# Kernel tuning notes

Hardware: AMD Instinct MI355X
Metric: run time of the kernel (lower is better)

Reference implementation:

```python
import jax, jax.numpy as jnp
import numpy as np

WS, OWS, HEADS, DIM = 16, 24, 6, 192
PAD = (OWS - WS) // 2
NQ, NKV = WS * WS, OWS * OWS
TABLE = (WS + OWS - 1) ** 2


def _rpi():
    # replicates WindowsHandling.get_relative_position_index_for_overlap_window
    c = np.arange(WS)
    ori = np.stack(np.meshgrid(c, c, indexing='ij')).reshape(2, -1)
    e = np.arange(OWS)
    ext = np.stack(np.meshgrid(e, e, indexing='ij')).reshape(2, -1)
    rc = (ext[:, None, :] - ori[:, :, None]).transpose(1, 2, 0).astype(np.int64)
    rc[..., 0] += WS - OWS + 1
    rc[..., 1] += WS - OWS + 1
    rc[..., 0] *= WS + OWS - 1
    # mod mimics torch's negative advanced-index wraparound into the table
    return (rc.sum(-1) % TABLE).astype(np.int32)  # (NQ, NKV)


def _extract_patches(xp, nh, nw):
    # torch.nn.Unfold(kernel=OWS, stride=WS) equivalent on NHWC input.
    # xp: (b, PH, PW, c) -> (b*nh*nw, OWS*OWS, c), row-major window order.
    b, PH, PW, c = xp.shape
    i = (np.arange(nh) * WS)[:, None] + np.arange(OWS)[None, :]
    j = (np.arange(nw) * WS)[:, None] + np.arange(OWS)[None, :]
    t = jnp.take(xp, jnp.asarray(i.reshape(-1)), axis=1).reshape(b, nh, OWS, PW, c)
    t = jnp.take(t, jnp.asarray(j.reshape(-1)), axis=3).reshape(b, nh, OWS, nw, OWS, c)
    return t.transpose(0, 1, 3, 2, 4, 5).reshape(b * nh * nw, OWS * OWS, c)


def _attn_mask(h, w):
    # shift_size == 0 branch of get_attention_mask_for_overlap_window:
    # kv positions falling into the zero padding get -100.
    vm = np.zeros((1, h + 2 * PAD, w + 2 * PAD, 1), np.float32)
    vm[:, PAD:-PAD, PAD:-PAD, :] = 1.0
    nh, nw = h // WS, w // WS
    kv = np.asarray(_extract_patches(jnp.asarray(vm), nh, nw)).reshape(nh * nw, NKV)
    m = np.where(kv[:, None, :] > 0, 0.0, -100.0).astype(np.float32)
    return np.broadcast_to(m, (nh * nw, NQ, NKV)).copy()


def setup_inputs():
    key = jax.random.key(0)
    ks = jax.random.split(key, 8)
    b, h, w = 2, 160, 160
    s = 0.02
    return {
        'x': jax.random.normal(ks[0], (b, h, w, DIM), jnp.float32),
        'rpi': jnp.asarray(_rpi()),
        'attn_mask': jnp.asarray(_attn_mask(h, w)),
        'q_w': jax.random.normal(ks[1], (DIM, DIM), jnp.float32) * s,
        'q_b': jnp.zeros((DIM,), jnp.float32),
        'kv_w': jax.random.normal(ks[2], (DIM, 2 * DIM), jnp.float32) * s,
        'kv_b': jnp.zeros((2 * DIM,), jnp.float32),
        'bias_table': jax.random.normal(ks[3], (TABLE, HEADS), jnp.float32) * s,
        'gating_w': jax.random.normal(ks[4], (DIM, DIM), jnp.float32) * s,
        'gating_b': jnp.ones((DIM,), jnp.float32),
        'proj_w': jax.random.normal(ks[5], (DIM, DIM), jnp.float32) * s,
        'proj_b': jnp.zeros((DIM,), jnp.float32),
    }


def reference(x, rpi, attn_mask, q_w, q_b, kv_w, kv_b, bias_table, gating_w, gating_b, proj_w, proj_b):
    b, h, w, c = x.shape
    d = c // HEADS
    scale = d ** -0.5
    nh, nw = h // WS, w // WS
    nwin = nh * nw
    # shift_size == 0 path: zero-pad for overlapping kv windows
    x_pad = jnp.pad(x, ((0, 0), (PAD, PAD), (PAD, PAD), (0, 0)))
    # q windows (non-overlapping window partition)
    xw = x.reshape(b, nh, WS, nw, WS, c).transpose(0, 1, 3, 2, 4, 5).reshape(b * nwin, NQ, c)
    # kv windows (overlapping, Unfold equivalent)
    xpw = _extract_patches(x_pad, nh, nw)  # (b*nwin, NKV, c)
    gates = xw @ gating_w + gating_b                       # (b*nwin, NQ, c)
    q = (xw @ q_w + q_b).reshape(-1, NQ, HEADS, d).transpose(0, 2, 1, 3) * scale
    kv = xpw @ kv_w + kv_b
    k = kv[..., :c].reshape(-1, NKV, HEADS, d).transpose(0, 2, 1, 3)
    v = kv[..., c:].reshape(-1, NKV, HEADS, d).transpose(0, 2, 1, 3)
    attn = jnp.einsum('bhqd,bhkd->bhqk', q, k)             # (b*nwin, H, NQ, NKV)
    bias = bias_table[rpi.reshape(-1)].reshape(NQ, NKV, HEADS).transpose(2, 0, 1)
    attn = attn + bias[None]
    attn = attn.reshape(b, nwin, HEADS, NQ, NKV) + attn_mask[None, :, None]
    attn = jax.nn.softmax(attn, axis=-1).reshape(b * nwin, HEADS, NQ, NKV)
    out = jnp.einsum('bhqk,bhkd->bhqd', attn, v).transpose(0, 2, 1, 3).reshape(-1, NQ, c)
    out = out * gates
    out = out.reshape(b, nh, nw, WS, WS, c).transpose(0, 1, 3, 2, 4, 5).reshape(b, h, w, c)
    return out @ proj_w + proj_b
```

## Files before the change

kernel.cpp:

```cpp
#include <hip/hip_runtime.h>
#include <hip/hip_bf16.h>
#include <stdint.h>

typedef __bf16 bf16x8  __attribute__((ext_vector_type(8)));
typedef __bf16 bf16x4  __attribute__((ext_vector_type(4)));
typedef __bf16 bf16x16 __attribute__((ext_vector_type(16)));
typedef float  f32x4   __attribute__((ext_vector_type(4)));
typedef float  f32x16  __attribute__((ext_vector_type(16)));
typedef uint32_t u32;

#define MFMA16(a, b, c) __builtin_amdgcn_mfma_f32_16x16x32_bf16((a), (b), (c), 0, 0, 0)
#define MFMA32(a, b, c) __builtin_amdgcn_mfma_f32_32x32x16_bf16((a), (b), (c), 0, 0, 0)

constexpr int CH = 160, CW = 160, CC = 192, CHEADS = 6, CD = 32;
constexpr int CNQ = 256, CNKV = 576, CPH = 168;
constexpr float LOG2E = 1.44269504088896340736f;
constexpr float QSCALE_L2E = 0.17677669529663687f * 1.44269504088896340736f;

__global__ __launch_bounds__(256)
void prep_k(const int* __restrict__ rpi, const float* __restrict__ tab,
            const float* __restrict__ q_w, const float* __restrict__ g_w,
            const float* __restrict__ kv_w, const float* __restrict__ p_w,
            const float* __restrict__ q_b, const float* __restrict__ g_b,
            const float* __restrict__ kv_b, const float* __restrict__ p_b,
            __bf16* __restrict__ BTh, u32* __restrict__ mt,
            __bf16* __restrict__ Wt, __bf16* __restrict__ Wp,
            float* __restrict__ b768, float* __restrict__ pb,
            __bf16* __restrict__ KVb)
{
    const int bidg = blockIdx.x;
    if (bidg < 216) {
        int idx = bidg * 256 + threadIdx.x;
        int lane = idx & 63;
        int rest = idx >> 6;
        int ktg = rest % 18; rest /= 18;
        int qtg = rest & 7;
        int head = rest >> 3;
        int l31 = lane & 31, hi = lane >> 5;
        int q = qtg * 32 + l31;
        bf16x16 o16;
#pragma unroll
        for (int g = 0; g < 4; ++g) {
            int4 ri = *(const int4*)(rpi + q * CNKV + ktg * 32 + 4 * hi + g * 8);
            o16[g * 4 + 0] = (__bf16)(tab[ri.x * CHEADS + head] * LOG2E);
            o16[g * 4 + 1] = (__bf16)(tab[ri.y * CHEADS + head] * LOG2E);
            o16[g * 4 + 2] = (__bf16)(tab[ri.z * CHEADS + head] * LOG2E);
            o16[g * 4 + 3] = (__bf16)(tab[ri.w * CHEADS + head] * LOG2E);
        }
        *(bf16x16*)(BTh + (long)idx * 16) = o16;
    } else if (bidg < 257) {
        int idx = (bidg - 216) * 256 + threadIdx.x;
        if (idx >= 9 * 18 * 64) return;
        int lane = idx & 63;
        int rest = idx >> 6;
        int ktg = rest % 18;
        int cls = rest / 18;
        int cy = cls / 3, cx = cls % 3;
        int hi = lane >> 5;
        u32 m = 0;
#pragma unroll
        for (int r = 0; r < 16; ++r) {
            int kv = ktg * 32 + 4 * hi + (r & 3) + 8 * (r >> 2);
            int oy = kv / 24, ox = kv - oy * 24;
            bool vy = (cy == 0) ? (oy >= 4) : ((cy == 2) ? (oy < 20) : true);
            bool vx = (cx == 0) ? (ox >= 4) : ((cx == 2) ? (ox < 20) : true);
            if (vy && vx) m |= (1u << r);
        }
        mt[idx] = m;
    } else if (bidg < 981) {
        int idx = (bidg - 257) * 256 + threadIdx.x;
        if (idx < 147456) {
            int n = idx / 192, k = idx - n * 192;
            float v;
            if (n < 192)      v = q_w[k * 192 + n] * QSCALE_L2E;
            else if (n < 384) v = g_w[k * 192 + (n - 192)];
            else              v = kv_w[k * 384 + (n - 384)];
            Wt[idx] = (__bf16)v;
        } else if (idx < 184320) {
            int j = idx - 147456;
            int n = j / 192, k = j - n * 192;
            Wp[j] = (__bf16)p_w[k * 192 + n];
        } else if (idx < 185280) {
            int j = idx - 184320;
            if (j < 192)      b768[j] = q_b[j] * QSCALE_L2E;
            else if (j < 384) b768[j] = g_b[j - 192];
            else if (j < 768) b768[j] = kv_b[j - 384];
            else              pb[j - 768] = p_b[j - 768];
        }
    } else {
        int tid = (bidg - 981) * 256 + threadIdx.x;
        if (tid >= 251904) return;
        int row = tid / 48, seg = tid - row * 48;
        int bb = row / 2624, rr = row - bb * 2624;
        int py, px;
        if (rr < 672)       { py = rr / 168;               px = rr % 168; }
        else if (rr < 1344) { int r2 = rr - 672; py = 164 + r2 / 168; px = r2 % 168; }
        else                { int rm = rr - 1344; py = 4 + rm / 8; int q = rm & 7;
                              px = (q < 4) ? q : 160 + q; }
        bf16x8 v;
#pragma unroll
        for (int j = 0; j < 8; ++j) v[j] = (__bf16)kv_b[seg * 8 + j];
        *(bf16x8*)(KVb + ((long)((bb * CPH + py) * CPH + px)) * 384 + seg * 8) = v;
    }
}

__global__ __launch_bounds__(256)
void gemm_f_k(const float* __restrict__ x, const __bf16* __restrict__ Wt,
              const float* __restrict__ b768,
              __bf16* __restrict__ Qb, __bf16* __restrict__ Gb,
              __bf16* __restrict__ KVb)
{
    __shared__ __bf16 As[2][4096];
    __shared__ __bf16 Bs[2][4096];

    const int bid = blockIdx.x;
    const int v = (bid & 7) * 1200 + (bid >> 3);
    const int bm = v / 12, bn = v - bm * 12;

    const int t = threadIdx.x, lane = t & 63, wv = t >> 6;
    const int l15 = lane & 15, l4 = lane >> 4;
    const int row = t >> 2, gp = t & 3;
    const int swz = row & 7;
    const int d0 = row * 64 + ((2 * gp) ^ swz) * 8;
    const int d1 = row * 64 + ((2 * gp + 1) ^ swz) * 8;

    const float*  asrc = x  + (long)(bm * 64 + row) * 192 + gp * 16;
    const __bf16* bsrc = Wt + (long)(bn * 64 + row) * 192 + gp * 16;

    float4 fa0, fa1, fa2, fa3;
    bf16x8 wb0, wb1;
    auto ld = [&](int kt) {
        const float* a = asrc + kt * 64;
        fa0 = ((const float4*)a)[0]; fa1 = ((const float4*)a)[1];
        fa2 = ((const float4*)a)[2]; fa3 = ((const float4*)a)[3];
        wb0 = *(const bf16x8*)(bsrc + kt * 64);
        wb1 = *(const bf16x8*)(bsrc + kt * 64 + 8);
    };
    auto st = [&](int buf) {
        bf16x8 g0, g1;
        g0[0] = (__bf16)fa0.x; g0[1] = (__bf16)fa0.y; g0[2] = (__bf16)fa0.z; g0[3] = (__bf16)fa0.w;
        g0[4] = (__bf16)fa1.x; g0[5] = (__bf16)fa1.y; g0[6] = (__bf16)fa1.z; g0[7] = (__bf16)fa1.w;
        g1[0] = (__bf16)fa2.x; g1[1] = (__bf16)fa2.y; g1[2] = (__bf16)fa2.z; g1[3] = (__bf16)fa2.w;
        g1[4] = (__bf16)fa3.x; g1[5] = (__bf16)fa3.y; g1[6] = (__bf16)fa3.z; g1[7] = (__bf16)fa3.w;
        *(bf16x8*)&As[buf][d0] = g0;
        *(bf16x8*)&As[buf][d1] = g1;
        *(bf16x8*)&Bs[buf][d0] = wb0;
        *(bf16x8*)&Bs[buf][d1] = wb1;
    };

    const int qm = (wv >> 1) * 32, qn = (wv & 1) * 32;
    f32x4 acc[2][2];
#pragma unroll
    for (int i = 0; i < 2; ++i)
#pragma unroll
        for (int j = 0; j < 2; ++j) acc[i][j] = f32x4{0.f, 0.f, 0.f, 0.f};

    ld(0);
    for (int kt = 0; kt < 3; ++kt) {
        const int buf = kt & 1;
        st(buf);
        if (kt < 2) ld(kt + 1);
        __syncthreads();
#pragma unroll
        for (int s = 0; s < 2; ++s) {
            bf16x8 af[2], bfr[2];
#pragma unroll
            for (int mi = 0; mi < 2; ++mi)
                af[mi] = *(const bf16x8*)&As[buf][(qm + mi * 16 + l15) * 64 +
                                                 (((s * 4 + l4) ^ (l15 & 7)) * 8)];
#pragma unroll
            for (int ni = 0; ni < 2; ++ni)
                bfr[ni] = *(const bf16x8*)&Bs[buf][(qn + ni * 16 + l15) * 64 +
                                                   (((s * 4 + l4) ^ (l15 & 7)) * 8)];
#pragma unroll
            for (int mi = 0; mi < 2; ++mi)
#pragma unroll
                for (int ni = 0; ni < 2; ++ni)
                    acc[mi][ni] = MFMA16(af[mi], bfr[ni], acc[mi][ni]);
        }
        __syncthreads();
    }

    __bf16* epi = &As[0][0];
    float bv0 = b768[bn * 64 + qn + l15];
    float bv1 = b768[bn * 64 + qn + 16 + l15];
#pragma unroll
    for (int mi = 0; mi < 2; ++mi)
#pragma unroll
        for (int ni = 0; ni < 2; ++ni)
#pragma unroll
            for (int r = 0; r < 4; ++r) {
                int rowl = qm + mi * 16 + l4 * 4 + r;
                int coll = qn + ni * 16 + l15;
                epi[rowl * 80 + coll] =
                    (__bf16)(acc[mi][ni][r] + (ni ? bv1 : bv0));
            }
    __syncthreads();
#pragma unroll
    for (int k = 0; k < 2; ++k) {
        int rid = t * 2 + k;
        int rowl = rid >> 3, seg = rid & 7;
        bf16x8 vv = *(const bf16x8*)&epi[rowl * 80 + seg * 8];
        int rowg = bm * 64 + rowl;
        int bb = rowg / 25600, rr = rowg - bb * 25600;
        int y = rr / 160, xx = rr - y * 160;
        int cg = bn * 64 + seg * 8;
        if (bn < 6) {
            int win = bb * 100 + (y >> 4) * 10 + (xx >> 4);
            long widx = ((long)win * 256 + (y & 15) * 16 + (xx & 15)) * 192;
            if (bn < 3) *(bf16x8*)(Qb + widx + cg) = vv;
            else        *(bf16x8*)(Gb + widx + cg - 192) = vv;
        } else {
            long kidx = ((long)((bb * CPH + y + 4) * CPH + (xx + 4))) * 384;
            *(bf16x8*)(KVb + kidx + cg - 384) = vv;
        }
    }
}

__global__ __launch_bounds__(256)
void gemm_p_k(const __bf16* __restrict__ Yb, const __bf16* __restrict__ Wp,
              const float* __restrict__ pb, float* __restrict__ of)
{
    __shared__ __bf16 As[2][4096];
    __shared__ __bf16 Bs[2][4096];

    const int bid = blockIdx.x;
    const int v = (bid & 7) * 300 + (bid >> 3);
    const int bm = v / 3, bn = v - bm * 3;

    const int t = threadIdx.x, lane = t & 63, wv = t >> 6;
    const int l15 = lane & 15, l4 = lane >> 4;
    const int row = t >> 2, gp = t & 3;
    const int swz = row & 7;
    const int d0 = row * 64 + ((2 * gp) ^ swz) * 8;
    const int d1 = row * 64 + ((2 * gp + 1) ^ swz) * 8;

    const __bf16* asrc = Yb + (long)(bm * 64 + row) * 192 + gp * 16;
    const __bf16* bsrc = Wp + (long)(bn * 64 + row) * 192 + gp * 16;

    bf16x8 a0, a1, wb0, wb1;
    auto ld = [&](int kt) {
        a0  = *(const bf16x8*)(asrc + kt * 64);
        a1  = *(const bf16x8*)(asrc + kt * 64 + 8);
        wb0 = *(const bf16x8*)(bsrc + kt * 64);
        wb1 = *(const bf16x8*)(bsrc + kt * 64 + 8);
    };
    auto st = [&](int buf) {
        *(bf16x8*)&As[buf][d0] = a0;
        *(bf16x8*)&As[buf][d1] = a1;
        *(bf16x8*)&Bs[buf][d0] = wb0;
        *(bf16x8*)&Bs[buf][d1] = wb1;
    };

    const int qm = (wv >> 1) * 32, qn = (wv & 1) * 32;
    f32x4 acc[2][2];
#pragma unroll
    for (int i = 0; i < 2; ++i)
#pragma unroll
        for (int j = 0; j < 2; ++j) acc[i][j] = f32x4{0.f, 0.f, 0.f, 0.f};

    ld(0);
    for (int kt = 0; kt < 3; ++kt) {
        const int buf = kt & 1;
        st(buf);
        if (kt < 2) ld(kt + 1);
        __syncthreads();
#pragma unroll
        for (int s = 0; s < 2; ++s) {
            bf16x8 af[2], bfr[2];
#pragma unroll
            for (int mi = 0; mi < 2; ++mi)
                af[mi] = *(const bf16x8*)&As[buf][(qm + mi * 16 + l15) * 64 +
                                                 (((s * 4 + l4) ^ (l15 & 7)) * 8)];
#pragma unroll
            for (int ni = 0; ni < 2; ++ni)
                bfr[ni] = *(const bf16x8*)&Bs[buf][(qn + ni * 16 + l15) * 64 +
                                                   (((s * 4 + l4) ^ (l15 & 7)) * 8)];
#pragma unroll
            for (int mi = 0; mi < 2; ++mi)
#pragma unroll
                for (int ni = 0; ni < 2; ++ni)
                    acc[mi][ni] = MFMA16(af[mi], bfr[ni], acc[mi][ni]);
        }
        __syncthreads();
    }

#pragma unroll
    for (int mi = 0; mi < 2; ++mi) {
#pragma unroll
        for (int r = 0; r < 4; ++r) {
            int rowg = bm * 64 + qm + mi * 16 + l4 * 4 + r;
            int win = rowg >> 8, q = rowg & 255;
            int bb = win / 100, wr = win % 100;
            int y = (wr / 10) * 16 + (q >> 4), xx = (wr % 10) * 16 + (q & 15);
            long oidx = ((long)((bb * CH + y) * CW + xx)) * 192;
#pragma unroll
            for (int ni = 0; ni < 2; ++ni) {
                int cg = bn * 64 + qn + ni * 16 + l15;
                of[oidx + cg] = acc[mi][ni][r] + pb[cg];
            }
        }
    }
}

__global__ __launch_bounds__(512, 4)
void attn12_k(const __bf16* __restrict__ Q, const __bf16* __restrict__ KV,
              const __bf16* __restrict__ G, const __bf16* __restrict__ BTh,
              const u32* __restrict__ MT, __bf16* __restrict__ Y)
{
    __shared__ __bf16 Ks[576][36];
    __shared__ __bf16 Vt[32][580];

    const int bid = blockIdx.x;
    const int xs = bid & 7, ii = bid >> 3;
    const int win = xs * 25 + ii / 6;
    const int head = ii % 6;

    const int bb = win / 100, wr = win % 100, wy = wr / 10, wx = wr % 10;
    const int cy = (wy == 0) ? 0 : ((wy == 9) ? 2 : 1);
    const int cx = (wx == 0) ? 0 : ((wx == 9) ? 2 : 1);
    const int cls = cy * 3 + cx;
    const int t = threadIdx.x, lane = t & 63, wv = t >> 6;
    const int l31 = lane & 31, hi = lane >> 5;

    {
        const int pos0 = t >> 3, seg = t & 7;
        int oy = pos0 / 24, ox = pos0 - oy * 24;
        const long rowbase = ((long)((bb * CPH + wy * 16) * CPH + wx * 16)) * 384
                             + head * CD;
        int pos = pos0;
#pragma unroll
        for (int r = 0; r < 9; ++r) {
            const __bf16* p = KV + rowbase + (long)(oy * CPH + ox) * 384;
            if (seg < 4) {
                bf16x8 k8 = *(const bf16x8*)(p + seg * 8);
                *(bf16x8*)&Ks[pos][seg * 8] = k8;
            } else {
                bf16x8 v8 = *(const bf16x8*)(p + 192 + (seg - 4) * 8);
#pragma unroll
                for (int j = 0; j < 8; ++j) Vt[(seg - 4) * 8 + j][pos] = v8[j];
            }
            pos += 64;
            oy += 2; ox += 16;
            if (ox >= 24) { ox -= 24; oy += 1; }
        }
    }

    bf16x8 qf0, qf1;
    {
        const __bf16* qb = Q + ((long)win * CNQ + wv * 32 + l31) * CC + head * CD;
        qf0 = *(const bf16x8*)(qb + hi * 8);
        qf1 = *(const bf16x8*)(qb + 16 + hi * 8);
    }
    const __bf16* btb = BTh + (long)((head * 8 + wv) * 18) * 1024 + (long)lane * 16;
    bf16x16 bA = *(const bf16x16*)btb;

    __syncthreads();

    f32x16 o = {};
    float srun = 0.f;

    const char* kbase = (const char*)&Ks[0][0] + l31 * 72 + hi * 16;
    const char* vbase = (const char*)&Vt[0][0] + l31 * 1160 + hi * 8;

    bf16x8 kc0 = *(const bf16x8*)(kbase);
    bf16x8 kc1 = *(const bf16x8*)(kbase + 32);
    f32x16 stv_cur;
#pragma unroll
    for (int r = 0; r < 16; ++r) stv_cur[r] = (float)bA[r];
    __builtin_amdgcn_s_setprio(1);
    stv_cur = MFMA32(kc0, qf0, stv_cur);
    stv_cur = MFMA32(kc1, qf1, stv_cur);
    __builtin_amdgcn_s_setprio(0);
    kc0 = *(const bf16x8*)(kbase + 2304);
    kc1 = *(const bf16x8*)(kbase + 2304 + 32);
    bA  = *(const bf16x16*)(btb + 1024);

    for (int tt = 0; tt < 18; ++tt) {
        f32x16 stv_next;
        if (tt < 17) {
#pragma unroll
            for (int r = 0; r < 16; ++r) stv_next[r] = (float)bA[r];
            __builtin_amdgcn_s_setprio(1);
            stv_next = MFMA32(kc0, qf0, stv_next);
            stv_next = MFMA32(kc1, qf1, stv_next);
            __builtin_amdgcn_s_setprio(0);
            if (tt < 16) {
                const char* kn = kbase + (tt + 2) * 2304;
                kc0 = *(const bf16x8*)(kn);
                kc1 = *(const bf16x8*)(kn + 32);
                bA  = *(const bf16x16*)(btb + (long)(tt + 2) * 1024);
            }
        }

        const char* vp = vbase + tt * 64;
        bf16x4 v0 = *(const bf16x4*)(vp);
        bf16x4 v1 = *(const bf16x4*)(vp + 16);
        bf16x4 v2 = *(const bf16x4*)(vp + 32);
        bf16x4 v3 = *(const bf16x4*)(vp + 48);
        bf16x8 vf0, vf1;
#pragma unroll
        for (int j = 0; j < 4; ++j) {
            vf0[j] = v0[j]; vf0[4 + j] = v1[j];
            vf1[j] = v2[j]; vf1[4 + j] = v3[j];
        }

        const bool needm = (cx != 1) || (cy == 0 && tt < 3) || (cy == 2 && tt >= 15);
        u32 m = 0xFFFFFFFFu;
        if (needm) m = MT[(cls * 18 + tt) * 64 + lane];

        float p[16];
#pragma unroll
        for (int r = 0; r < 16; ++r) p[r] = exp2f(stv_cur[r]);
        if (needm) {
#pragma unroll
            for (int r = 0; r < 16; ++r)
                p[r] = (m & (1u << r)) ? p[r] : 0.0f;
        }
        float s = 0.f;
#pragma unroll
        for (int r = 0; r < 16; ++r) s += p[r];
        srun += s;

        bf16x8 pa0, pa1;
#pragma unroll
        for (int j = 0; j < 8; ++j) {
            pa0[j] = (__bf16)p[j];
            pa1[j] = (__bf16)p[8 + j];
        }

        __builtin_amdgcn_s_setprio(1);
        o = MFMA32(vf0, pa0, o);
        o = MFMA32(vf1, pa1, o);
        __builtin_amdgcn_s_setprio(0);

        if (tt < 17) stv_cur = stv_next;
    }

    srun += __shfl_xor(srun, 32);
    float rs = 1.0f / srun;
    long base = ((long)win * CNQ + wv * 32 + l31) * CC + head * CD;
    const __bf16* gp2 = G + base;
    __bf16* yp = Y + base;
#pragma unroll
    for (int g = 0; g < 4; ++g) {
        bf16x4 gv = *(const bf16x4*)(gp2 + g * 8 + 4 * hi);
        bf16x4 ov;
#pragma unroll
        for (int j = 0; j < 4; ++j)
            ov[j] = (__bf16)(o[g * 4 + j] * rs * (float)gv[j]);
        *(bf16x4*)(yp + g * 8 + 4 * hi) = ov;
    }
}

extern "C" void kernel_launch(void* const* d_in, const int* in_sizes, int n_in,
                              void* d_out, int out_size, void* d_ws, size_t ws_size,
                              hipStream_t stream)
{
    (void)in_sizes; (void)n_in; (void)out_size; (void)ws_size;
    const float* x    = (const float*)d_in[0];
    const int*   rpi  = (const int*)  d_in[1];
    const float* q_w  = (const float*)d_in[3];
    const float* q_b  = (const float*)d_in[4];
    const float* kv_w = (const float*)d_in[5];
    const float* kv_b = (const float*)d_in[6];
    const float* btab = (const float*)d_in[7];
    const float* g_w  = (const float*)d_in[8];
    const float* g_b  = (const float*)d_in[9];
    const float* p_w  = (const float*)d_in[10];
    const float* p_b  = (const float*)d_in[11];
    float* out = (float*)d_out;

    char* ws = (char*)d_ws;
    __bf16* Qb  = (__bf16*)(ws);
    __bf16* KVb = (__bf16*)(ws + 19660800);
    __bf16* Gb  = (__bf16*)(ws + 63012864);
    __bf16* Yb  = (__bf16*)(ws + 82673664);
    __bf16* BTh = (__bf16*)(ws + 102334464);
    u32*    MT  = (u32*)   (ws + 104103936);
    __bf16* Wt  = (__bf16*)(ws + 104145408);
    __bf16* Wp  = (__bf16*)(ws + 104440320);
    float*  b768= (float*) (ws + 104514048);
    float*  pb  = (float*) (ws + 104517120);

    prep_k<<<1965, 256, 0, stream>>>(rpi, btab, q_w, g_w, kv_w, p_w,
                                     q_b, g_b, kv_b, p_b,
                                     BTh, MT, Wt, Wp, b768, pb, KVb);
    gemm_f_k<<<9600, 256, 0, stream>>>(x, Wt, b768, Qb, Gb, KVb);
    attn12_k<<<1200, 512, 0, stream>>>(Qb, KVb, Gb, BTh, MT, Yb);
    gemm_p_k<<<2400, 256, 0, stream>>>(Yb, Wp, pb, out);
}
```

Before: 144.8 us.

## Enlarge fused GEMM M-tile, restructure attention loop, sum probabilities via MFMA

The fused Q/gate/KV projection GEMM now uses 128x64 tiles instead of 64x64, halving the block count and increasing reuse of the weight tile per block. The attention kernel drops the one-step-ahead score pipelining in favour of prefetching only the next K and bias loads. Row sums of the probabilities are now accumulated with extra MFMAs against a ones vector instead of scalar adds plus a cross-lane shuffle. exp2f is swapped for the hardware builtin when available. The changes add register pressure and extra MFMA work, and may expose score latency that the old pipelining hid.

```diff
diff --git a/kernel.cpp b/kernel.cpp
--- a/kernel.cpp
+++ b/kernel.cpp
@@ -11,6 +11,12 @@
 
 #define MFMA16(a, b, c) __builtin_amdgcn_mfma_f32_16x16x32_bf16((a), (b), (c), 0, 0, 0)
 #define MFMA32(a, b, c) __builtin_amdgcn_mfma_f32_32x32x16_bf16((a), (b), (c), 0, 0, 0)
+
+#if __has_builtin(__builtin_amdgcn_exp2f)
+#define EXP2F(x) __builtin_amdgcn_exp2f(x)
+#else
+#define EXP2F(x) exp2f(x)
+#endif
 
 constexpr int CH = 160, CW = 160, CC = 192, CHEADS = 6, CD = 32;
 constexpr int CNQ = 256, CNKV = 576, CPH = 168;
@@ -110,48 +116,51 @@
               __bf16* __restrict__ Qb, __bf16* __restrict__ Gb,
               __bf16* __restrict__ KVb)
 {
-    __shared__ __bf16 As[2][4096];
+    __shared__ __bf16 As[2][8192];
     __shared__ __bf16 Bs[2][4096];
 
     const int bid = blockIdx.x;
-    const int v = (bid & 7) * 1200 + (bid >> 3);
+    const int v = (bid & 7) * 600 + (bid >> 3);
     const int bm = v / 12, bn = v - bm * 12;
 
     const int t = threadIdx.x, lane = t & 63, wv = t >> 6;
     const int l15 = lane & 15, l4 = lane >> 4;
-    const int row = t >> 2, gp = t & 3;
-    const int swz = row & 7;
-    const int d0 = row * 64 + ((2 * gp) ^ swz) * 8;
-    const int d1 = row * 64 + ((2 * gp + 1) ^ swz) * 8;
-
-    const float*  asrc = x  + (long)(bm * 64 + row) * 192 + gp * 16;
-    const __bf16* bsrc = Wt + (long)(bn * 64 + row) * 192 + gp * 16;
-
-    float4 fa0, fa1, fa2, fa3;
+    const int wm = wv >> 1, wn = wv & 1;
+
+    const int arow = t >> 1, ahalf = t & 1;
+    const int aswz = arow & 7;
+    const int brow = t >> 2, bgp = t & 3;
+    const int bswz = brow & 7;
+
+    const float*  asrc = x  + (long)(bm * 128 + arow) * 192 + ahalf * 32;
+    const __bf16* bsrc = Wt + (long)(bn * 64 + brow) * 192 + bgp * 16;
+
+    float4 fa[8];
     bf16x8 wb0, wb1;
     auto ld = [&](int kt) {
         const float* a = asrc + kt * 64;
-        fa0 = ((const float4*)a)[0]; fa1 = ((const float4*)a)[1];
-        fa2 = ((const float4*)a)[2]; fa3 = ((const float4*)a)[3];
+#pragma unroll
+        for (int q = 0; q < 8; ++q) fa[q] = ((const float4*)a)[q];
         wb0 = *(const bf16x8*)(bsrc + kt * 64);
         wb1 = *(const bf16x8*)(bsrc + kt * 64 + 8);
     };
     auto st = [&](int buf) {
-        bf16x8 g0, g1;
-        g0[0] = (__bf16)fa0.x; g0[1] = (__bf16)fa0.y; g0[2] = (__bf16)fa0.z; g0[3] = (__bf16)fa0.w;
-        g0[4] = (__bf16)fa1.x; g0[5] = (__bf16)fa1.y; g0[6] = (__bf16)fa1.z; g0[7] = (__bf16)fa1.w;
-        g1[0] = (__bf16)fa2.x; g1[1] = (__bf16)fa2.y; g1[2] = (__bf16)fa2.z; g1[3] = (__bf16)fa2.w;
-        g1[4] = (__bf16)fa3.x; g1[5] = (__bf16)fa3.y; g1[6] = (__bf16)fa3.z; g1[7] = (__bf16)fa3.w;
-        *(bf16x8*)&As[buf][d0] = g0;
-        *(bf16x8*)&As[buf][d1] = g1;
-        *(bf16x8*)&Bs[buf][d0] = wb0;
-        *(bf16x8*)&Bs[buf][d1] = wb1;
+#pragma unroll
+        for (int c = 0; c < 4; ++c) {
+            bf16x8 g;
+            g[0] = (__bf16)fa[2 * c].x; g[1] = (__bf16)fa[2 * c].y;
+            g[2] = (__bf16)fa[2 * c].z; g[3] = (__bf16)fa[2 * c].w;
+            g[4] = (__bf16)fa[2 * c + 1].x; g[5] = (__bf16)fa[2 * c + 1].y;
+            g[6] = (__bf16)fa[2 * c + 1].z; g[7] = (__bf16)fa[2 * c + 1].w;
+            *(bf16x8*)&As[buf][arow * 64 + ((ahalf * 4 + c) ^ aswz) * 8] = g;
+        }
+        *(bf16x8*)&Bs[buf][brow * 64 + ((2 * bgp) ^ bswz) * 8] = wb0;
+        *(bf16x8*)&Bs[buf][brow * 64 + ((2 * bgp + 1) ^ bswz) * 8] = wb1;
     };
 
-    const int qm = (wv >> 1) * 32, qn = (wv & 1) * 32;
-    f32x4 acc[2][2];
-#pragma unroll
-    for (int i = 0; i < 2; ++i)
+    f32x4 acc[4][2];
+#pragma unroll
+    for (int i = 0; i < 4; ++i)
 #pragma unroll
         for (int j = 0; j < 2; ++j) acc[i][j] = f32x4{0.f, 0.f, 0.f, 0.f};
 
@@ -163,17 +172,17 @@
         __syncthreads();
 #pragma unroll
         for (int s = 0; s < 2; ++s) {
-            bf16x8 af[2], bfr[2];
-#pragma unroll
-            for (int mi = 0; mi < 2; ++mi)
-                af[mi] = *(const bf16x8*)&As[buf][(qm + mi * 16 + l15) * 64 +
+            bf16x8 af[4], bfr[2];
+#pragma unroll
+            for (int mi = 0; mi < 4; ++mi)
+                af[mi] = *(const bf16x8*)&As[buf][(wm * 64 + mi * 16 + l15) * 64 +
                                                  (((s * 4 + l4) ^ (l15 & 7)) * 8)];
 #pragma unroll
             for (int ni = 0; ni < 2; ++ni)
-                bfr[ni] = *(const bf16x8*)&Bs[buf][(qn + ni * 16 + l15) * 64 +
+                bfr[ni] = *(const bf16x8*)&Bs[buf][(wn * 32 + ni * 16 + l15) * 64 +
                                                    (((s * 4 + l4) ^ (l15 & 7)) * 8)];
 #pragma unroll
-            for (int mi = 0; mi < 2; ++mi)
+            for (int mi = 0; mi < 4; ++mi)
 #pragma unroll
                 for (int ni = 0; ni < 2; ++ni)
                     acc[mi][ni] = MFMA16(af[mi], bfr[ni], acc[mi][ni]);
@@ -182,26 +191,26 @@
     }
 
     __bf16* epi = &As[0][0];
-    float bv0 = b768[bn * 64 + qn + l15];
-    float bv1 = b768[bn * 64 + qn + 16 + l15];
-#pragma unroll
-    for (int mi = 0; mi < 2; ++mi)
+    float bv0 = b768[bn * 64 + wn * 32 + l15];
+    float bv1 = b768[bn * 64 + wn * 32 + 16 + l15];
+#pragma unroll
+    for (int mi = 0; mi < 4; ++mi)
 #pragma unroll
         for (int ni = 0; ni < 2; ++ni)
 #pragma unroll
             for (int r = 0; r < 4; ++r) {
-                int rowl = qm + mi * 16 + l4 * 4 + r;
-                int coll = qn + ni * 16 + l15;
+                int rowl = wm * 64 + mi * 16 + l4 * 4 + r;
+                int coll = wn * 32 + ni * 16 + l15;
                 epi[rowl * 80 + coll] =
                     (__bf16)(acc[mi][ni][r] + (ni ? bv1 : bv0));
             }
     __syncthreads();
 #pragma unroll
-    for (int k = 0; k < 2; ++k) {
-        int rid = t * 2 + k;
+    for (int k = 0; k < 4; ++k) {
+        int rid = k * 256 + t;
         int rowl = rid >> 3, seg = rid & 7;
         bf16x8 vv = *(const bf16x8*)&epi[rowl * 80 + seg * 8];
-        int rowg = bm * 64 + rowl;
+        int rowg = bm * 128 + rowl;
         int bb = rowg / 25600, rr = rowg - bb * 25600;
         int y = rr / 160, xx = rr - y * 160;
         int cg = bn * 64 + seg * 8;
@@ -304,7 +313,7 @@
 }
 
 __global__ __launch_bounds__(512, 4)
-void attn12_k(const __bf16* __restrict__ Q, const __bf16* __restrict__ KV,
+void attn13_k(const __bf16* __restrict__ Q, const __bf16* __restrict__ KV,
               const __bf16* __restrict__ G, const __bf16* __restrict__ BTh,
               const u32* __restrict__ MT, __bf16* __restrict__ Y)
 {
@@ -355,42 +364,29 @@
     const __bf16* btb = BTh + (long)((head * 8 + wv) * 18) * 1024 + (long)lane * 16;
     bf16x16 bA = *(const bf16x16*)btb;
 
+    bf16x8 ones8;
+#pragma unroll
+    for (int j = 0; j < 8; ++j) ones8[j] = (__bf16)1.0f;
+
     __syncthreads();
 
     f32x16 o = {};
-    float srun = 0.f;
+    f32x16 sacc = {};
 
     const char* kbase = (const char*)&Ks[0][0] + l31 * 72 + hi * 16;
     const char* vbase = (const char*)&Vt[0][0] + l31 * 1160 + hi * 8;
 
     bf16x8 kc0 = *(const bf16x8*)(kbase);
     bf16x8 kc1 = *(const bf16x8*)(kbase + 32);
-    f32x16 stv_cur;
-#pragma unroll
-    for (int r = 0; r < 16; ++r) stv_cur[r] = (float)bA[r];
-    __builtin_amdgcn_s_setprio(1);
-    stv_cur = MFMA32(kc0, qf0, stv_cur);
-    stv_cur = MFMA32(kc1, qf1, stv_cur);
-    __builtin_amdgcn_s_setprio(0);
-    kc0 = *(const bf16x8*)(kbase + 2304);
-    kc1 = *(const bf16x8*)(kbase + 2304 + 32);
-    bA  = *(const bf16x16*)(btb + 1024);
 
     for (int tt = 0; tt < 18; ++tt) {
-        f32x16 stv_next;
+        bf16x8 kn0, kn1;
+        bf16x16 bB;
         if (tt < 17) {
-#pragma unroll
-            for (int r = 0; r < 16; ++r) stv_next[r] = (float)bA[r];
-            __builtin_amdgcn_s_setprio(1);
-            stv_next = MFMA32(kc0, qf0, stv_next);
-            stv_next = MFMA32(kc1, qf1, stv_next);
-            __builtin_amdgcn_s_setprio(0);
-            if (tt < 16) {
-                const char* kn = kbase + (tt + 2) * 2304;
-                kc0 = *(const bf16x8*)(kn);
-                kc1 = *(const bf16x8*)(kn + 32);
-                bA  = *(const bf16x16*)(btb + (long)(tt + 2) * 1024);
-            }
+            const char* kn = kbase + (tt + 1) * 2304;
+            kn0 = *(const bf16x8*)(kn);
+            kn1 = *(const bf16x8*)(kn + 32);
+            bB  = *(const bf16x16*)(btb + (long)(tt + 1) * 1024);
         }
 
         const char* vp = vbase + tt * 64;
@@ -405,22 +401,26 @@
             vf1[j] = v2[j]; vf1[4 + j] = v3[j];
         }
 
+        f32x16 stv;
+#pragma unroll
+        for (int r = 0; r < 16; ++r) stv[r] = (float)bA[r];
+        __builtin_amdgcn_s_setprio(1);
+        stv = MFMA32(kc0, qf0, stv);
+        stv = MFMA32(kc1, qf1, stv);
+        __builtin_amdgcn_s_setprio(0);
+
         const bool needm = (cx != 1) || (cy == 0 && tt < 3) || (cy == 2 && tt >= 15);
         u32 m = 0xFFFFFFFFu;
         if (needm) m = MT[(cls * 18 + tt) * 64 + lane];
 
         float p[16];
 #pragma unroll
-        for (int r = 0; r < 16; ++r) p[r] = exp2f(stv_cur[r]);
+        for (int r = 0; r < 16; ++r) p[r] = EXP2F(stv[r]);
         if (needm) {
 #pragma unroll
             for (int r = 0; r < 16; ++r)
                 p[r] = (m & (1u << r)) ? p[r] : 0.0f;
         }
-        float s = 0.f;
-#pragma unroll
-        for (int r = 0; r < 16; ++r) s += p[r];
-        srun += s;
 
         bf16x8 pa0, pa1;
 #pragma unroll
@@ -432,13 +432,14 @@
         __builtin_amdgcn_s_setprio(1);
         o = MFMA32(vf0, pa0, o);
         o = MFMA32(vf1, pa1, o);
+        sacc = MFMA32(ones8, pa0, sacc);
+        sacc = MFMA32(ones8, pa1, sacc);
         __builtin_amdgcn_s_setprio(0);
 
-        if (tt < 17) stv_cur = stv_next;
-    }
-
-    srun += __shfl_xor(srun, 32);
-    float rs = 1.0f / srun;
+        kc0 = kn0; kc1 = kn1; bA = bB;
+    }
+
+    float rs = 1.0f / sacc[0];
     long base = ((long)win * CNQ + wv * 32 + l31) * CC + head * CD;
     const __bf16* gp2 = G + base;
     __bf16* yp = Y + base;
@@ -486,7 +487,7 @@
     prep_k<<<1965, 256, 0, stream>>>(rpi, btab, q_w, g_w, kv_w, p_w,
                                      q_b, g_b, kv_b, p_b,
                                      BTh, MT, Wt, Wp, b768, pb, KVb);
-    gemm_f_k<<<9600, 256, 0, stream>>>(x, Wt, b768, Qb, Gb, KVb);
-    attn12_k<<<1200, 512, 0, stream>>>(Qb, KVb, Gb, BTh, MT, Yb);
+    gemm_f_k<<<4800, 256, 0, stream>>>(x, Wt, b768, Qb, Gb, KVb);
+    attn13_k<<<1200, 512, 0, stream>>>(Qb, KVb, Gb, BTh, MT, Yb);
     gemm_p_k<<<2400, 256, 0, stream>>>(Yb, Wp, pb, out);
 }
```

After: 155.9 us. 7.7% more time.
